# Performance work log

Hardware: AMD Instinct MI355X
Metric: run time of the kernel (lower is better)

Reference implementation:

```python
import jax, jax.numpy as jnp
import numpy as np

B, C, W, H, HEADS = 4, 512, 32, 32, 8
D = C // HEADS          # head dim = 64
N = W * H               # tokens = 1024


def setup_inputs() -> dict:
    key = jax.random.key(0)
    ks = jax.random.split(key, 11)
    s = 0.02
    return {
        "q1": jax.random.normal(ks[0], (B, C, W, H), jnp.float32),
        "q2": jax.random.normal(ks[1], (B, C, W, H), jnp.float32),
        "q3": jax.random.normal(ks[2], (B, C, W, H), jnp.float32),
        "Wq": jax.random.normal(ks[3], (C, C), jnp.float32) * s,
        "bq": jnp.zeros((C,), jnp.float32),
        "Wk": jax.random.normal(ks[4], (C, C), jnp.float32) * s,
        "bk": jnp.zeros((C,), jnp.float32),
        "Wv": jax.random.normal(ks[5], (C, C), jnp.float32) * s,
        "bv": jnp.zeros((C,), jnp.float32),
        # BoT-style relative position embeddings (broadcast over the grid)
        "rel_h": jax.random.normal(ks[6], (HEADS, D, 1, H), jnp.float32) * s,
        "rel_w": jax.random.normal(ks[7], (HEADS, D, W, 1), jnp.float32) * s,
    }


def reference(q1, q2, q3, Wq, bq, Wk, bk, Wv, bv, rel_h, rel_w):
    b, c, w, h = q1.shape
    heads = rel_h.shape[0]
    d = c // heads
    n = w * h

    def proj(x, Wm, bm):
        # 1x1 conv == channel matmul; then view (b, heads, d, n)
        y = jnp.einsum('oc,bchw->bohw', Wm, x) + bm[None, :, None, None]
        return y.reshape(b, heads, d, n)

    q = proj(q1, Wq, bq)
    k = proj(q2, Wk, bk)
    v = proj(q3, Wv, bv)

    # (heads, d, w, h) -> (heads, d, n); used transposed as (heads, n, d)
    pos = (rel_h + rel_w).reshape(heads, d, n)

    def branch(a, bmat, outv):
        # energy = a^T bmat + pos^T a ; softmax over last dim; out = outv @ attn^T
        energy = (jnp.einsum('bhdn,bhdm->bhnm', a, bmat)
                  + jnp.einsum('hdn,bhdm->bhnm', pos, a))
        attn = jax.nn.softmax(energy, axis=-1)  # (b, heads, n, n)
        out = jnp.einsum('bhdm,bhnm->bhdn', outv, attn)
        return out.reshape(b, c, w, h)

    out_q = branch(q, k, v)   # energy_q = q^T k + pos^T q ; out = v @ attn_q^T
    out_k = branch(k, v, q)   # energy_k = k^T v + pos^T k ; out = q @ attn_k^T
    out_v = branch(v, q, k)   # energy_v = v^T q + pos^T v ; out = k @ attn_v^T

    return jnp.concatenate((out_q, out_k, out_v), axis=0)
```

## Files before the change

### kernel.cpp

```cpp
#include <hip/hip_runtime.h>

typedef __attribute__((ext_vector_type(8))) __bf16 bf16x8;
typedef __attribute__((ext_vector_type(4))) float f32x4;
typedef __attribute__((ext_vector_type(4))) int i32x4;
typedef __attribute__((ext_vector_type(2))) int i32x2;
typedef __attribute__((ext_vector_type(4))) unsigned short u16x4;
typedef __attribute__((ext_vector_type(8))) unsigned short u16x8;
typedef unsigned short u16;
typedef unsigned int u32;

#define DEVI __device__ __forceinline__

constexpr int CB = 4;
constexpr int CC = 512;
constexpr int CH = 8;
constexpr int CD = 64;
constexpr int CN = 1024;
constexpr float L2E = 1.44269504088896f;

DEVI u16 f2bf(float f) {
    u32 u = __builtin_bit_cast(u32, f);
    u = (u + 0x7FFFu + ((u >> 16) & 1u)) >> 16;
    return (u16)u;
}
DEVI float bf2f(u16 u) {
    return __builtin_bit_cast(float, (u32)u << 16);
}
DEVI u16 f2bf_c(float f) {
    return __builtin_bit_cast(u16, (__bf16)f);
}
DEVI float exp2_fast(float x) {
    float r;
    asm("v_exp_f32 %0, %1" : "=v"(r) : "v"(x));
    return r;
}

DEVI int swzA(int row, int col16) {
    return (row * 256 + col16 * 16) ^ ((row & 7) << 4);
}
DEVI int swzB(int row, int col16) {
    return (row * 128 + col16 * 16) ^ ((row & 7) << 4);
}

DEVI bf16x8 ldfrag(const u16* base, int byteoff) {
    const i32x4* p = reinterpret_cast<const i32x4*>(reinterpret_cast<const char*>(base) + byteoff);
    return __builtin_bit_cast(bf16x8, *p);
}
DEVI void st16(u16* base, int byteoff, i32x4 v) {
    *reinterpret_cast<i32x4*>(reinterpret_cast<char*>(base) + byteoff) = v;
}
DEVI void st8(u16* base, int byteoff, i32x2 v) {
    *reinterpret_cast<i32x2*>(reinterpret_cast<char*>(base) + byteoff) = v;
}
DEVI void async16(u16* lds, const u16* g) {
    __builtin_amdgcn_global_load_lds(
        (const __attribute__((address_space(1))) unsigned int*)g,
        (__attribute__((address_space(3))) unsigned int*)lds,
        16, 0, 0);
}

__global__ __launch_bounds__(256) void mqf_convx_kernel(
    const float* __restrict__ q1, const float* __restrict__ q2, const float* __restrict__ q3,
    const float* __restrict__ Wq, const float* __restrict__ Wk, const float* __restrict__ Wv,
    u16* __restrict__ XT, u16* __restrict__ Wbf)
{
    __shared__ u16 T[64 * 66];
    const int t = threadIdx.x;
    const int n0 = blockIdx.x * 64, c0 = blockIdx.y * 64;
    const int p = blockIdx.z >> 2, b = blockIdx.z & 3;
    const float* X = (p == 0 ? q1 : p == 1 ? q2 : q3) + (size_t)b * CC * CN;
    u16* dst = XT + (size_t)(p * CB + b) * CN * CC;

    if (t < 128) {
        int bid = blockIdx.x + (blockIdx.y << 4) + (blockIdx.z << 7);
        int idx = (bid * 128 + t) * 4;
        int pw = idx >> 18;
        int off = idx & 0x3FFFF;
        const float* W = (pw == 0 ? Wq : pw == 1 ? Wk : Wv);
        f32x4 v = *reinterpret_cast<const f32x4*>(W + off);
        u16x4 pk;
        #pragma unroll
        for (int j = 0; j < 4; ++j) pk[j] = f2bf(v[j]);
        *reinterpret_cast<u16x4*>(Wbf + idx) = pk;
    }

    #pragma unroll
    for (int pass = 0; pass < 4; ++pass) {
        int idx = pass * 256 + t;
        int cl = idx >> 4, nl = (idx & 15) * 4;
        f32x4 v = *reinterpret_cast<const f32x4*>(X + (size_t)(c0 + cl) * CN + n0 + nl);
        u32 lo = (u32)f2bf(v[0]) | ((u32)f2bf(v[1]) << 16);
        u32 hi = (u32)f2bf(v[2]) | ((u32)f2bf(v[3]) << 16);
        *reinterpret_cast<u32*>(&T[cl * 66 + nl]) = lo;
        *reinterpret_cast<u32*>(&T[cl * 66 + nl + 2]) = hi;
    }
    __syncthreads();
    #pragma unroll
    for (int pass = 0; pass < 2; ++pass) {
        int idx = pass * 256 + t;
        int nl = idx >> 3, g = idx & 7;
        u16x8 pk;
        #pragma unroll
        for (int j = 0; j < 8; ++j) pk[j] = T[(g * 8 + j) * 66 + nl];
        *reinterpret_cast<u16x8*>(dst + (size_t)(n0 + nl) * CC + c0 + g * 8) = pk;
    }
}

__global__ __launch_bounds__(256) void mqf_gemm_kernel(
    const u16* __restrict__ Wbf, const u16* __restrict__ XT,
    const float* __restrict__ bq, const float* __restrict__ bk, const float* __restrict__ bv,
    u16* __restrict__ projN, u16* __restrict__ projT)
{
    __shared__ __align__(16) u16 At[128 * 64];
    __shared__ __align__(16) u16 Bt[128 * 64];

    const int t = threadIdx.x;
    const int w = t >> 6, l = t & 63;
    const int n0 = blockIdx.x * 128;
    const int o0 = blockIdx.y * 128;
    const int p = blockIdx.z >> 2, b = blockIdx.z & 3;

    const u16* A = Wbf + (size_t)p * CC * CC;
    const u16* B = XT + (size_t)(p * CB + b) * CN * CC;
    const float* bm = (p == 0 ? bq : p == 1 ? bk : bv);
    u16* oN = projN + (size_t)(p * CB + b) * CC * CN;
    u16* oT = projT + (size_t)(p * CB + b) * CN * CC;

    const int srow = t >> 3;
    const int sj = t & 7;

    const f32x4 fz = {0.f, 0.f, 0.f, 0.f};
    f32x4 acc[4][4];
    #pragma unroll
    for (int m = 0; m < 4; ++m)
        #pragma unroll
        for (int s = 0; s < 4; ++s) acc[m][s] = fz;

    const int wr = (w >> 1) * 64;
    const int wc = (w & 1) * 64;

    for (int c0 = 0; c0 < CC; c0 += 64) {
        __syncthreads();
        #pragma unroll
        for (int q = 0; q < 4; ++q) {
            int row = q * 32 + srow;
            int col = (sj ^ (row & 7)) * 8;
            async16(&At[q * 2048 + t * 8], A + (size_t)(o0 + row) * CC + c0 + col);
            async16(&Bt[q * 2048 + t * 8], B + (size_t)(n0 + row) * CC + c0 + col);
        }
        __syncthreads();
        __builtin_amdgcn_s_setprio(1);
        #pragma unroll
        for (int kk = 0; kk < 2; ++kk) {
            bf16x8 af[4], bfr[4];
            #pragma unroll
            for (int m = 0; m < 4; ++m)
                af[m] = ldfrag(At, swzB(wr + m * 16 + (l & 15), kk * 4 + (l >> 4)));
            #pragma unroll
            for (int s = 0; s < 4; ++s)
                bfr[s] = ldfrag(Bt, swzB(wc + s * 16 + (l & 15), kk * 4 + (l >> 4)));
            #pragma unroll
            for (int m = 0; m < 4; ++m)
                #pragma unroll
                for (int s = 0; s < 4; ++s)
                    acc[m][s] = __builtin_amdgcn_mfma_f32_16x16x32_bf16(af[m], bfr[s], acc[m][s], 0, 0, 0);
        }
        __builtin_amdgcn_s_setprio(0);
    }

    #pragma unroll
    for (int m = 0; m < 4; ++m) {
        int obase = o0 + wr + m * 16 + (l >> 4) * 4;
        float bias[4];
        #pragma unroll
        for (int r = 0; r < 4; ++r) bias[r] = bm[obase + r];
        #pragma unroll
        for (int s = 0; s < 4; ++s) {
            int n = n0 + wc + s * 16 + (l & 15);
            u16x4 pk;
            #pragma unroll
            for (int r = 0; r < 4; ++r) {
                float v = acc[m][s][r] + bias[r];
                pk[r] = f2bf(v);
                oN[(size_t)(obase + r) * CN + n] = pk[r];
            }
            *reinterpret_cast<u16x4*>(oT + (size_t)n * CC + obase) = pk;
        }
    }
}

__global__ __launch_bounds__(256, 3) void mqf_attn_kernel(
    const u16* __restrict__ projN, const u16* __restrict__ projT,
    const float* __restrict__ rel_h, const float* __restrict__ rel_w,
    float* __restrict__ out)
{
    __shared__ __align__(16) u16 Kt[2][64 * 128];
    __shared__ __align__(16) u16 Vt[2][64 * 64];

    const int t = threadIdx.x;
    const int w = t >> 6, l = t & 63;
    const int li = l & 15, hi = l >> 4;

    int id = blockIdx.x + (blockIdx.y << 3) + (blockIdx.z << 8);
    int nid = (id & 7) * 96 + (id >> 3);
    const int n0 = (nid & 7) * 128;
    const int by = (nid >> 3) & 31;
    const int br = nid >> 8;
    const int b = by >> 3, h = by & 7;

    const int ai = br, bi = (br + 1) % 3, vi = (br + 2) % 3;
    const size_t tsz = (size_t)CB * CC * CN;
    const u16* aT = projT + ai * tsz + (size_t)b * CN * CC;
    const u16* bT = projT + bi * tsz + (size_t)b * CN * CC;
    const u16* vN = projN + vi * tsz + (size_t)b * CC * CN;

    bf16x8 qf[2][4];
    #pragma unroll
    for (int g = 0; g < 2; ++g) {
        const int nq = n0 + (w * 2 + g) * 16 + li;
        #pragma unroll
        for (int kk = 0; kk < 2; ++kk) {
            u16x8 raw = *reinterpret_cast<const u16x8*>(
                aT + (size_t)nq * CC + h * CD + kk * 32 + hi * 8);
            u16x8 pk;
            #pragma unroll
            for (int j = 0; j < 8; ++j) pk[j] = f2bf_c(bf2f(raw[j]) * L2E);
            qf[g][kk] = __builtin_bit_cast(bf16x8, pk);
        }
        #pragma unroll
        for (int kk = 2; kk < 4; ++kk) {
            u16x8 pk;
            #pragma unroll
            for (int j = 0; j < 8; ++j) {
                int d = (kk - 2) * 32 + hi * 8 + j;
                float f = rel_h[(h * CD + d) * 32 + (nq & 31)]
                        + rel_w[(h * CD + d) * 32 + (nq >> 5)];
                pk[j] = f2bf_c(f * L2E);
            }
            qf[g][kk] = __builtin_bit_cast(bf16x8, pk);
        }
    }

    const f32x4 fz = {0.f, 0.f, 0.f, 0.f};
    f32x4 oacc[2][4];
    #pragma unroll
    for (int g = 0; g < 2; ++g)
        #pragma unroll
        for (int dg = 0; dg < 4; ++dg) oacc[g][dg] = fz;
    float lsum[2] = {0.f, 0.f};

    i32x4 vreg[2];
    const int vrow = t >> 3, vc = (t & 7) * 8;
    const int vb0 = ((vc >> 5) << 6) + (((vc >> 2) & 3) << 4) + (((vc >> 4) & 1) << 3);

    auto loadV = [&](int m1) {
        const u16* rv = vN + (size_t)(h * CD + vrow) * CN + m1;
        vreg[0] = *reinterpret_cast<const i32x4*>(rv + vc);
        vreg[1] = *reinterpret_cast<const i32x4*>(rv + (size_t)32 * CN + vc);
    };
    auto writeV = [&](u16* VtW) {
        i32x2 lo0 = {vreg[0][0], vreg[0][1]}, hi0 = {vreg[0][2], vreg[0][3]};
        int r0 = vrow, r1 = vrow + 32;
        st8(VtW, (r0 * 128 + vb0) ^ ((r0 & 7) << 4), lo0);
        st8(VtW, (r0 * 128 + vb0 + 16) ^ ((r0 & 7) << 4), hi0);
        i32x2 lo1 = {vreg[1][0], vreg[1][1]}, hi1 = {vreg[1][2], vreg[1][3]};
        st8(VtW, (r1 * 128 + vb0) ^ ((r1 & 7) << 4), lo1);
        st8(VtW, (r1 * 128 + vb0 + 16) ^ ((r1 & 7) << 4), hi1);
    };
    auto issueKdma = [&](int m1, u16* KtW) {
        #pragma unroll
        for (int i = 0; i < 4; ++i) {
            int row = w * 16 + i * 4 + hi;
            int col16 = li ^ (row & 7);
            const u16* src = ((li & 8) ? aT : bT)
                + (size_t)(m1 + row) * CC + h * CD + (col16 & 7) * 8;
            async16(KtW + w * 2048 + i * 512 + l * 8, src);
        }
    };

    loadV(0);
    writeV(Vt[0]);
    issueKdma(0, Kt[0]);
    loadV(64);
    __syncthreads();

    for (int tt = 0; tt < 16; ++tt) {
        if (tt < 15) {
            writeV(Vt[(tt + 1) & 1]);
            issueKdma((tt + 1) * 64, Kt[(tt + 1) & 1]);
        }
        if (tt < 14) loadV((tt + 2) * 64);

        const u16* KtC = Kt[tt & 1];
        const u16* VtC = Vt[tt & 1];

        f32x4 e[2][4];
        #pragma unroll
        for (int s = 0; s < 4; ++s) { e[0][s] = fz; e[1][s] = fz; }
        __builtin_amdgcn_s_setprio(1);
        #pragma unroll
        for (int kk = 0; kk < 4; ++kk) {
            #pragma unroll
            for (int s = 0; s < 4; ++s) {
                bf16x8 af = ldfrag(KtC, swzA(s * 16 + li, kk * 4 + hi));
                e[0][s] = __builtin_amdgcn_mfma_f32_16x16x32_bf16(af, qf[0][kk], e[0][s], 0, 0, 0);
                e[1][s] = __builtin_amdgcn_mfma_f32_16x16x32_bf16(af, qf[1][kk], e[1][s], 0, 0, 0);
            }
        }
        __builtin_amdgcn_s_setprio(0);

        bf16x8 pa[2][2];
        #pragma unroll
        for (int g = 0; g < 2; ++g) {
            float ts = 0.f;
            #pragma unroll
            for (int s = 0; s < 4; ++s) {
                #pragma unroll
                for (int r = 0; r < 4; ++r) {
                    float pv = exp2_fast(e[g][s][r]);
                    e[g][s][r] = pv;
                    ts += pv;
                }
            }
            lsum[g] += ts;
            #pragma unroll
            for (int kk = 0; kk < 2; ++kk) {
                u16x8 pk;
                #pragma unroll
                for (int r = 0; r < 4; ++r) {
                    pk[r]     = f2bf_c(e[g][2 * kk][r]);
                    pk[4 + r] = f2bf_c(e[g][2 * kk + 1][r]);
                }
                pa[g][kk] = __builtin_bit_cast(bf16x8, pk);
            }
        }

        __builtin_amdgcn_s_setprio(1);
        #pragma unroll
        for (int kk = 0; kk < 2; ++kk) {
            #pragma unroll
            for (int dg = 0; dg < 4; ++dg) {
                bf16x8 vf = ldfrag(VtC, swzB(dg * 16 + li, kk * 4 + hi));
                oacc[0][dg] = __builtin_amdgcn_mfma_f32_16x16x32_bf16(vf, pa[0][kk], oacc[0][dg], 0, 0, 0);
                oacc[1][dg] = __builtin_amdgcn_mfma_f32_16x16x32_bf16(vf, pa[1][kk], oacc[1][dg], 0, 0, 0);
            }
        }
        __builtin_amdgcn_s_setprio(0);
        __syncthreads();
    }

    #pragma unroll
    for (int g = 0; g < 2; ++g) {
        float lt = lsum[g];
        lt += __shfl_xor(lt, 16, 64);
        lt += __shfl_xor(lt, 32, 64);
        float inv = 1.f / lt;
        float* outp = out + ((size_t)(br * CB + b) * CC + h * CD) * CN
                    + n0 + (w * 2 + g) * 16 + li;
        #pragma unroll
        for (int dg = 0; dg < 4; ++dg) {
            #pragma unroll
            for (int r = 0; r < 4; ++r) {
                int drow = dg * 16 + hi * 4 + r;
                outp[(size_t)drow * CN] = oacc[g][dg][r] * inv;
            }
        }
    }
}

extern "C" void kernel_launch(void* const* d_in, const int* in_sizes, int n_in,
                              void* d_out, int out_size, void* d_ws, size_t ws_size,
                              hipStream_t stream) {
    const float* q1 = (const float*)d_in[0];
    const float* q2 = (const float*)d_in[1];
    const float* q3 = (const float*)d_in[2];
    const float* Wq = (const float*)d_in[3];
    const float* bq = (const float*)d_in[4];
    const float* Wk = (const float*)d_in[5];
    const float* bk = (const float*)d_in[6];
    const float* Wv = (const float*)d_in[7];
    const float* bv = (const float*)d_in[8];
    const float* rh = (const float*)d_in[9];
    const float* rw = (const float*)d_in[10];

    u16* XT    = (u16*)d_ws;
    u16* Wbf   = XT + (size_t)3 * CB * CN * CC;
    u16* projN = Wbf + (size_t)3 * CC * CC;
    u16* projT = projN + (size_t)3 * CB * CC * CN;
    float* outp = (float*)d_out;

    dim3 gc(CN / 64, CC / 64, 12);
    mqf_convx_kernel<<<gc, 256, 0, stream>>>(q1, q2, q3, Wq, Wk, Wv, XT, Wbf);
    dim3 gg(CN / 128, CC / 128, 12);
    mqf_gemm_kernel<<<gg, 256, 0, stream>>>(Wbf, XT, bq, bk, bv, projN, projT);
    dim3 ga(CN / 128, CB * CH, 3);
    mqf_attn_kernel<<<ga, 256, 0, stream>>>(projN, projT, rh, rw, outp);
}
```

Baseline: 75.72 us.

## Double-buffer projection GEMM, stage epilogue through LDS, split attention softmax/PV

The projection GEMM switches to 64x128 tiles with a double-buffered async LDS pipeline, so the next K-slice loads while the current one computes. Block IDs are remapped, and the epilogue stages fp32 results through LDS so both the normal and transposed bf16 outputs are written as coalesced 16-byte stores. The attention inner loop is split in two halves, so the exp/convert of the second half can overlap with the PV MFMAs of the first half. This doubles the GEMM grid, uses more LDS per block, and reshapes the attention instruction schedule.

Measured after the change: 72.58 us, median of 2. 4.1% less time.

```diff
diff --git a/kernel.cpp b/kernel.cpp
--- a/kernel.cpp
+++ b/kernel.cpp
@@ -45,9 +45,6 @@
 DEVI bf16x8 ldfrag(const u16* base, int byteoff) {
     const i32x4* p = reinterpret_cast<const i32x4*>(reinterpret_cast<const char*>(base) + byteoff);
     return __builtin_bit_cast(bf16x8, *p);
-}
-DEVI void st16(u16* base, int byteoff, i32x4 v) {
-    *reinterpret_cast<i32x4*>(reinterpret_cast<char*>(base) + byteoff) = v;
 }
 DEVI void st8(u16* base, int byteoff, i32x2 v) {
     *reinterpret_cast<i32x2*>(reinterpret_cast<char*>(base) + byteoff) = v;
@@ -111,14 +108,23 @@
     const float* __restrict__ bq, const float* __restrict__ bk, const float* __restrict__ bv,
     u16* __restrict__ projN, u16* __restrict__ projT)
 {
-    __shared__ __align__(16) u16 At[128 * 64];
-    __shared__ __align__(16) u16 Bt[128 * 64];
+    __shared__ __align__(16) char lds_raw[49152];
+    u16* At0 = (u16*)lds_raw;
+    u16* At1 = At0 + 4096;
+    u16* Bt0 = At0 + 8192;
+    u16* Bt1 = Bt0 + 8192;
+    float* Tb = (float*)lds_raw;
 
     const int t = threadIdx.x;
     const int w = t >> 6, l = t & 63;
-    const int n0 = blockIdx.x * 128;
-    const int o0 = blockIdx.y * 128;
-    const int p = blockIdx.z >> 2, b = blockIdx.z & 3;
+    const int li = l & 15, hi = l >> 4;
+
+    int id = blockIdx.x + (blockIdx.y << 3) + (blockIdx.z << 6);
+    int nid = (id & 7) * 96 + (id >> 3);
+    const int n0 = (nid & 7) * 128;
+    const int o0 = ((nid >> 3) & 7) * 64;
+    const int pb = nid >> 6;
+    const int p = pb >> 2, b = pb & 3;
 
     const u16* A = Wbf + (size_t)p * CC * CC;
     const u16* B = XT + (size_t)(p * CB + b) * CN * CC;
@@ -126,65 +132,89 @@
     u16* oN = projN + (size_t)(p * CB + b) * CC * CN;
     u16* oT = projT + (size_t)(p * CB + b) * CN * CC;
 
-    const int srow = t >> 3;
     const int sj = t & 7;
 
+    auto issueDMA = [&](int step, u16* AtW, u16* BtW) {
+        int c0 = step * 64;
+        #pragma unroll
+        for (int q = 0; q < 2; ++q) {
+            int idx = q * 256 + t;
+            int row = idx >> 3;
+            int col = (sj ^ (row & 7)) * 8;
+            async16(AtW + idx * 8, A + (size_t)(o0 + row) * CC + c0 + col);
+        }
+        #pragma unroll
+        for (int q = 0; q < 4; ++q) {
+            int idx = q * 256 + t;
+            int row = idx >> 3;
+            int col = (sj ^ (row & 7)) * 8;
+            async16(BtW + idx * 8, B + (size_t)(n0 + row) * CC + c0 + col);
+        }
+    };
+
     const f32x4 fz = {0.f, 0.f, 0.f, 0.f};
-    f32x4 acc[4][4];
+    f32x4 acc[4][2];
     #pragma unroll
     for (int m = 0; m < 4; ++m)
         #pragma unroll
-        for (int s = 0; s < 4; ++s) acc[m][s] = fz;
-
-    const int wr = (w >> 1) * 64;
-    const int wc = (w & 1) * 64;
-
-    for (int c0 = 0; c0 < CC; c0 += 64) {
-        __syncthreads();
-        #pragma unroll
-        for (int q = 0; q < 4; ++q) {
-            int row = q * 32 + srow;
-            int col = (sj ^ (row & 7)) * 8;
-            async16(&At[q * 2048 + t * 8], A + (size_t)(o0 + row) * CC + c0 + col);
-            async16(&Bt[q * 2048 + t * 8], B + (size_t)(n0 + row) * CC + c0 + col);
-        }
-        __syncthreads();
+        for (int s = 0; s < 2; ++s) acc[m][s] = fz;
+
+    issueDMA(0, At0, Bt0);
+    __syncthreads();
+
+    for (int step = 0; step < 8; ++step) {
+        u16* AtC = (step & 1) ? At1 : At0;
+        u16* BtC = (step & 1) ? Bt1 : Bt0;
+        if (step < 7) issueDMA(step + 1, (step & 1) ? At0 : At1, (step & 1) ? Bt0 : Bt1);
+
         __builtin_amdgcn_s_setprio(1);
         #pragma unroll
         for (int kk = 0; kk < 2; ++kk) {
-            bf16x8 af[4], bfr[4];
+            bf16x8 af[4], bfr[2];
             #pragma unroll
             for (int m = 0; m < 4; ++m)
-                af[m] = ldfrag(At, swzB(wr + m * 16 + (l & 15), kk * 4 + (l >> 4)));
-            #pragma unroll
-            for (int s = 0; s < 4; ++s)
-                bfr[s] = ldfrag(Bt, swzB(wc + s * 16 + (l & 15), kk * 4 + (l >> 4)));
+                af[m] = ldfrag(AtC, swzB(m * 16 + li, kk * 4 + hi));
+            #pragma unroll
+            for (int s = 0; s < 2; ++s)
+                bfr[s] = ldfrag(BtC, swzB(w * 32 + s * 16 + li, kk * 4 + hi));
             #pragma unroll
             for (int m = 0; m < 4; ++m)
                 #pragma unroll
-                for (int s = 0; s < 4; ++s)
+                for (int s = 0; s < 2; ++s)
                     acc[m][s] = __builtin_amdgcn_mfma_f32_16x16x32_bf16(af[m], bfr[s], acc[m][s], 0, 0, 0);
         }
         __builtin_amdgcn_s_setprio(0);
+        __syncthreads();
     }
 
     #pragma unroll
     for (int m = 0; m < 4; ++m) {
-        int obase = o0 + wr + m * 16 + (l >> 4) * 4;
-        float bias[4];
-        #pragma unroll
-        for (int r = 0; r < 4; ++r) bias[r] = bm[obase + r];
-        #pragma unroll
-        for (int s = 0; s < 4; ++s) {
-            int n = n0 + wc + s * 16 + (l & 15);
-            u16x4 pk;
-            #pragma unroll
-            for (int r = 0; r < 4; ++r) {
-                float v = acc[m][s][r] + bias[r];
-                pk[r] = f2bf(v);
-                oN[(size_t)(obase + r) * CN + n] = pk[r];
-            }
-            *reinterpret_cast<u16x4*>(oT + (size_t)n * CC + obase) = pk;
+        #pragma unroll
+        for (int r = 0; r < 4; ++r) {
+            int orow = m * 16 + hi * 4 + r;
+            float bias = bm[o0 + orow];
+            #pragma unroll
+            for (int s = 0; s < 2; ++s)
+                Tb[orow * 129 + w * 32 + s * 16 + li] = acc[m][s][r] + bias;
+        }
+    }
+    __syncthreads();
+    {
+        int row = t >> 2, nbase = (t & 3) * 32;
+        #pragma unroll
+        for (int j = 0; j < 4; ++j) {
+            u16x8 pk;
+            #pragma unroll
+            for (int i = 0; i < 8; ++i) pk[i] = f2bf_c(Tb[row * 129 + nbase + j * 8 + i]);
+            *reinterpret_cast<u16x8*>(oN + (size_t)(o0 + row) * CN + n0 + nbase + j * 8) = pk;
+        }
+        int nrow = t >> 1, obase = (t & 1) * 32;
+        #pragma unroll
+        for (int j = 0; j < 4; ++j) {
+            u16x8 pk;
+            #pragma unroll
+            for (int i = 0; i < 8; ++i) pk[i] = f2bf_c(Tb[(obase + j * 8 + i) * 129 + nrow]);
+            *reinterpret_cast<u16x8*>(oT + (size_t)(n0 + nrow) * CC + o0 + obase + j * 8) = pk;
         }
     }
 }
@@ -301,49 +331,68 @@
         #pragma unroll
         for (int kk = 0; kk < 4; ++kk) {
             #pragma unroll
-            for (int s = 0; s < 4; ++s) {
+            for (int s = 0; s < 2; ++s) {
                 bf16x8 af = ldfrag(KtC, swzA(s * 16 + li, kk * 4 + hi));
                 e[0][s] = __builtin_amdgcn_mfma_f32_16x16x32_bf16(af, qf[0][kk], e[0][s], 0, 0, 0);
                 e[1][s] = __builtin_amdgcn_mfma_f32_16x16x32_bf16(af, qf[1][kk], e[1][s], 0, 0, 0);
             }
         }
+        #pragma unroll
+        for (int kk = 0; kk < 4; ++kk) {
+            #pragma unroll
+            for (int s = 2; s < 4; ++s) {
+                bf16x8 af = ldfrag(KtC, swzA(s * 16 + li, kk * 4 + hi));
+                e[0][s] = __builtin_amdgcn_mfma_f32_16x16x32_bf16(af, qf[0][kk], e[0][s], 0, 0, 0);
+                e[1][s] = __builtin_amdgcn_mfma_f32_16x16x32_bf16(af, qf[1][kk], e[1][s], 0, 0, 0);
+            }
+        }
         __builtin_amdgcn_s_setprio(0);
 
-        bf16x8 pa[2][2];
+        bf16x8 pa0[2], pa1[2];
         #pragma unroll
         for (int g = 0; g < 2; ++g) {
             float ts = 0.f;
-            #pragma unroll
-            for (int s = 0; s < 4; ++s) {
-                #pragma unroll
-                for (int r = 0; r < 4; ++r) {
-                    float pv = exp2_fast(e[g][s][r]);
-                    e[g][s][r] = pv;
-                    ts += pv;
-                }
+            u16x8 pk;
+            #pragma unroll
+            for (int r = 0; r < 4; ++r) {
+                float p0 = exp2_fast(e[g][0][r]);
+                float p1 = exp2_fast(e[g][1][r]);
+                ts += p0 + p1;
+                pk[r] = f2bf_c(p0);
+                pk[4 + r] = f2bf_c(p1);
             }
             lsum[g] += ts;
-            #pragma unroll
-            for (int kk = 0; kk < 2; ++kk) {
-                u16x8 pk;
-                #pragma unroll
-                for (int r = 0; r < 4; ++r) {
-                    pk[r]     = f2bf_c(e[g][2 * kk][r]);
-                    pk[4 + r] = f2bf_c(e[g][2 * kk + 1][r]);
-                }
-                pa[g][kk] = __builtin_bit_cast(bf16x8, pk);
-            }
-        }
-
+            pa0[g] = __builtin_bit_cast(bf16x8, pk);
+        }
         __builtin_amdgcn_s_setprio(1);
         #pragma unroll
-        for (int kk = 0; kk < 2; ++kk) {
-            #pragma unroll
-            for (int dg = 0; dg < 4; ++dg) {
-                bf16x8 vf = ldfrag(VtC, swzB(dg * 16 + li, kk * 4 + hi));
-                oacc[0][dg] = __builtin_amdgcn_mfma_f32_16x16x32_bf16(vf, pa[0][kk], oacc[0][dg], 0, 0, 0);
-                oacc[1][dg] = __builtin_amdgcn_mfma_f32_16x16x32_bf16(vf, pa[1][kk], oacc[1][dg], 0, 0, 0);
-            }
+        for (int dg = 0; dg < 4; ++dg) {
+            bf16x8 vf = ldfrag(VtC, swzB(dg * 16 + li, hi));
+            oacc[0][dg] = __builtin_amdgcn_mfma_f32_16x16x32_bf16(vf, pa0[0], oacc[0][dg], 0, 0, 0);
+            oacc[1][dg] = __builtin_amdgcn_mfma_f32_16x16x32_bf16(vf, pa0[1], oacc[1][dg], 0, 0, 0);
+        }
+        __builtin_amdgcn_s_setprio(0);
+        #pragma unroll
+        for (int g = 0; g < 2; ++g) {
+            float ts = 0.f;
+            u16x8 pk;
+            #pragma unroll
+            for (int r = 0; r < 4; ++r) {
+                float p0 = exp2_fast(e[g][2][r]);
+                float p1 = exp2_fast(e[g][3][r]);
+                ts += p0 + p1;
+                pk[r] = f2bf_c(p0);
+                pk[4 + r] = f2bf_c(p1);
+            }
+            lsum[g] += ts;
+            pa1[g] = __builtin_bit_cast(bf16x8, pk);
+        }
+        __builtin_amdgcn_s_setprio(1);
+        #pragma unroll
+        for (int dg = 0; dg < 4; ++dg) {
+            bf16x8 vf = ldfrag(VtC, swzB(dg * 16 + li, 4 + hi));
+            oacc[0][dg] = __builtin_amdgcn_mfma_f32_16x16x32_bf16(vf, pa1[0], oacc[0][dg], 0, 0, 0);
+            oacc[1][dg] = __builtin_amdgcn_mfma_f32_16x16x32_bf16(vf, pa1[1], oacc[1][dg], 0, 0, 0);
         }
         __builtin_amdgcn_s_setprio(0);
         __syncthreads();
@@ -391,7 +440,7 @@
 
     dim3 gc(CN / 64, CC / 64, 12);
     mqf_convx_kernel<<<gc, 256, 0, stream>>>(q1, q2, q3, Wq, Wk, Wv, XT, Wbf);
-    dim3 gg(CN / 128, CC / 128, 12);
+    dim3 gg(CN / 128, CC / 64, 12);
     mqf_gemm_kernel<<<gg, 256, 0, stream>>>(Wbf, XT, bq, bk, bv, projN, projT);
     dim3 ga(CN / 128, CB * CH, 3);
     mqf_attn_kernel<<<ga, 256, 0, stream>>>(projN, projT, rh, rw, outp);
```
